# Kernel tuning notes

Hardware: AMD Instinct MI355X
Metric: run time of the kernel (lower is better)

Reference implementation:

```python
import jax, jax.numpy as jnp
import numpy as np

BETA = 1.0 - 0.01      # 1 - voltage_decay
THRESH = 1.0           # threshold_voltage; theta state is never updated in the
                       # original forward (theta1/theta2 stay at init=0), so the
                       # effective adaptive threshold is THRESH + 0 every step.
ALPHA = 2.0            # snntorch default ATan surrogate alpha

@jax.custom_vjp
def spike_fn(x):
    # Heaviside forward, ATan surrogate backward (snntorch default spike_grad)
    return (x > 0).astype(x.dtype)

def _spike_fwd(x):
    return (x > 0).astype(x.dtype), x

def _spike_bwd(x, g):
    return (g * (ALPHA / 2.0) / (1.0 + (jnp.pi / 2.0 * ALPHA * x) ** 2),)

spike_fn.defvjp(_spike_fwd, _spike_bwd)

def setup_inputs() -> dict:
    key = jax.random.key(0)
    k0, k1, k2 = jax.random.split(key, 3)
    B, T, D, H, A = 128, 32, 6400, 1000, 4
    x = jax.random.normal(k0, (B, T, D), jnp.float32)
    W1 = jax.random.normal(k1, (H, D), jnp.float32) * (1.0 / np.sqrt(D))
    b1 = jnp.zeros((H,), jnp.float32)
    W2 = jax.random.normal(k2, (A, H), jnp.float32) * (1.0 / np.sqrt(H))
    b2 = jnp.zeros((A,), jnp.float32)
    return {"x": x, "W1": W1, "b1": b1, "W2": W2, "b2": b2}

def _lif_step(mem, cur, thr):
    # snntorch Leaky, reset_mechanism='zero':
    #   reset based on PREVIOUS mem crossing threshold (detached),
    #   zeroes the whole new state (leaked mem + input) on reset step.
    reset = jax.lax.stop_gradient((mem > thr).astype(mem.dtype))
    mem_new = (BETA * mem + cur) * (1.0 - reset)
    spk = spike_fn(mem_new - thr)
    return spk, mem_new

def _snn_forward(x, W1, b1, W2, b2):
    B, T, _ = x.shape
    H, A = W1.shape[0], W2.shape[0]

    def step(carry, cur):
        mem1, mem2 = carry
        h1 = cur @ W1.T + b1                 # [B,H]
        spk1, mem1 = _lif_step(mem1, h1, THRESH)
        h2 = spk1 @ W2.T + b2                # [B,A]
        spk2, mem2 = _lif_step(mem2, h2, THRESH)
        return (mem1, mem2), spk2

    init = (jnp.zeros((B, H), x.dtype), jnp.zeros((B, A), x.dtype))
    xt = jnp.swapaxes(x, 0, 1)               # [T,B,D]
    _, spk2_rec = jax.lax.scan(step, init, xt)
    return jnp.swapaxes(spk2_rec, 0, 1)      # [B,T,A]

def reference(x, W1, b1, W2, b2):
    return _snn_forward(x, W1, b1, W2, b2)
```

## Files before the change

### kernel.cpp

```cpp
#include <hip/hip_runtime.h>
#include <hip/hip_bf16.h>

constexpr int Bn = 128;
constexpr int Tn = 32;
constexpr int Dn = 6400;
constexpr int Hn = 1000;
constexpr int An = 4;
constexpr int Mn = Bn * Tn;

typedef _Float16 half8 __attribute__((ext_vector_type(8)));
typedef float floatx4 __attribute__((ext_vector_type(4)));

__global__ __launch_bounds__(256, 4)
void gemm_split16(const float* __restrict__ X, const float* __restrict__ W1,
                  const float* __restrict__ b1, float* __restrict__ H1)
{
    constexpr int K = Dn;
    constexpr int LD = 72;
    __shared__ __align__(16) _Float16 As[2][64][LD];
    __shared__ __align__(16) _Float16 Bs[2][64][LD];

    const int tid = threadIdx.x;
    const int bm = blockIdx.x * 64;
    const int bn = blockIdx.y * 64;
    const int lane = tid & 63;
    const int wid = tid >> 6;
    const int wm = (wid & 1) * 32;
    const int wn = (wid >> 1) * 32;
    const int fr = lane & 15;
    const int fq = lane >> 4;

    const int row0 = tid >> 3;
    const int row1 = (tid + 256) >> 3;
    const int k8_0 = (tid & 7) * 8;
    const int k8_1 = k8_0;

    float4 rx[2][2], rw[2][2];
    const float zero4[4] = {0.f, 0.f, 0.f, 0.f};

    auto load_tiles = [&](int k0) {
        rx[0][0] = *(const float4*)(X + (size_t)(bm + row0) * K + k0 + k8_0);
        rx[0][1] = *(const float4*)(X + (size_t)(bm + row0) * K + k0 + k8_0 + 4);
        rx[1][0] = *(const float4*)(X + (size_t)(bm + row1) * K + k0 + k8_1);
        rx[1][1] = *(const float4*)(X + (size_t)(bm + row1) * K + k0 + k8_1 + 4);
        const int n0 = bn + row0, n1 = bn + row1;
        if (n0 < Hn) {
            rw[0][0] = *(const float4*)(W1 + (size_t)n0 * K + k0 + k8_0);
            rw[0][1] = *(const float4*)(W1 + (size_t)n0 * K + k0 + k8_0 + 4);
        } else { rw[0][0] = *(const float4*)zero4; rw[0][1] = *(const float4*)zero4; }
        if (n1 < Hn) {
            rw[1][0] = *(const float4*)(W1 + (size_t)n1 * K + k0 + k8_1);
            rw[1][1] = *(const float4*)(W1 + (size_t)n1 * K + k0 + k8_1 + 4);
        } else { rw[1][0] = *(const float4*)zero4; rw[1][1] = *(const float4*)zero4; }
    };

    load_tiles(0);

    floatx4 acc0[2][2] = {};
    floatx4 acc1[2][2] = {};

    for (int k0 = 0; k0 < K; k0 += 64) {
#pragma unroll
        for (int p = 0; p < 2; ++p) {
            const int row = p ? row1 : row0;
            const int k8 = p ? k8_1 : k8_0;
            float v[8];
            *(float4*)&v[0] = rx[p][0]; *(float4*)&v[4] = rx[p][1];
            half8 hi, lo;
#pragma unroll
            for (int j = 0; j < 8; ++j) {
                hi[j] = (_Float16)v[j];
                lo[j] = (_Float16)((v[j] - (float)hi[j]) * 4096.0f);
            }
            *(half8*)&As[0][row][k8] = hi;
            *(half8*)&As[1][row][k8] = lo;

            *(float4*)&v[0] = rw[p][0]; *(float4*)&v[4] = rw[p][1];
#pragma unroll
            for (int j = 0; j < 8; ++j) {
                hi[j] = (_Float16)v[j];
                lo[j] = (_Float16)((v[j] - (float)hi[j]) * 4096.0f);
            }
            *(half8*)&Bs[0][row][k8] = hi;
            *(half8*)&Bs[1][row][k8] = lo;
        }
        __syncthreads();

        if (k0 + 64 < K) load_tiles(k0 + 64);

#pragma unroll
        for (int c = 0; c < 2; ++c) {
            half8 ahi[2], alo[2], bhi[2], blo[2];
#pragma unroll
            for (int mt = 0; mt < 2; ++mt) {
                ahi[mt] = *(const half8*)&As[0][wm + mt * 16 + fr][c * 32 + fq * 8];
                alo[mt] = *(const half8*)&As[1][wm + mt * 16 + fr][c * 32 + fq * 8];
            }
#pragma unroll
            for (int nt = 0; nt < 2; ++nt) {
                bhi[nt] = *(const half8*)&Bs[0][wn + nt * 16 + fr][c * 32 + fq * 8];
                blo[nt] = *(const half8*)&Bs[1][wn + nt * 16 + fr][c * 32 + fq * 8];
            }
#pragma unroll
            for (int mt = 0; mt < 2; ++mt)
#pragma unroll
                for (int nt = 0; nt < 2; ++nt) {
                    acc0[mt][nt] = __builtin_amdgcn_mfma_f32_16x16x32_f16(ahi[mt], bhi[nt], acc0[mt][nt], 0, 0, 0);
                    acc1[mt][nt] = __builtin_amdgcn_mfma_f32_16x16x32_f16(ahi[mt], blo[nt], acc1[mt][nt], 0, 0, 0);
                    acc1[mt][nt] = __builtin_amdgcn_mfma_f32_16x16x32_f16(alo[mt], bhi[nt], acc1[mt][nt], 0, 0, 0);
                }
        }
        __syncthreads();
    }

#pragma unroll
    for (int nt = 0; nt < 2; ++nt) {
        const int n = bn + wn + nt * 16 + fr;
        if (n >= Hn) continue;
        const float bias = b1[n];
#pragma unroll
        for (int mt = 0; mt < 2; ++mt) {
            const int m = bm + wm + mt * 16 + fq * 4;
#pragma unroll
            for (int r = 0; r < 4; ++r)
                H1[(size_t)(m + r) * Hn + n] =
                    acc0[mt][nt][r] + acc1[mt][nt][r] * (1.0f / 4096.0f) + bias;
        }
    }
}

__global__ __launch_bounds__(1024)
void snn_scan(const float* __restrict__ H1, const float* __restrict__ W2,
              const float* __restrict__ b2, float* __restrict__ out)
{
    const int b = blockIdx.x;
    const int tid = threadIdx.x;
    const int lane = tid & 63;
    const int wid = tid >> 6;
    const bool act = (tid < Hn);

    float cur[Tn];
#pragma unroll
    for (int t = 0; t < Tn; ++t)
        cur[t] = act ? H1[((size_t)b * Tn + t) * Hn + tid] : 0.f;

    float w2[An];
#pragma unroll
    for (int a = 0; a < An; ++a)
        w2[a] = act ? W2[a * Hn + tid] : 0.f;

    __shared__ float red[16][An];
    float mem1 = 0.f;
    float mem2[An] = {0.f, 0.f, 0.f, 0.f};

    for (int t = 0; t < Tn; ++t) {
        const float reset = (mem1 > 1.0f) ? 1.0f : 0.0f;
        mem1 = (0.99f * mem1 + cur[t]) * (1.0f - reset);
        const bool spk = (mem1 > 1.0f);

        float p[An];
#pragma unroll
        for (int a = 0; a < An; ++a) p[a] = spk ? w2[a] : 0.f;

#pragma unroll
        for (int off = 32; off > 0; off >>= 1)
#pragma unroll
            for (int a = 0; a < An; ++a) p[a] += __shfl_down(p[a], off, 64);
        if (lane == 0) {
#pragma unroll
            for (int a = 0; a < An; ++a) red[wid][a] = p[a];
        }
        __syncthreads();

        if (wid == 0) {
            float q[An];
#pragma unroll
            for (int a = 0; a < An; ++a) q[a] = (lane < 16) ? red[lane][a] : 0.f;
#pragma unroll
            for (int off = 8; off > 0; off >>= 1)
#pragma unroll
                for (int a = 0; a < An; ++a) q[a] += __shfl_down(q[a], off, 64);
            if (lane == 0) {
#pragma unroll
                for (int a = 0; a < An; ++a) {
                    const float h2 = q[a] + b2[a];
                    const float reset2 = (mem2[a] > 1.0f) ? 1.0f : 0.0f;
                    const float m2 = (0.99f * mem2[a] + h2) * (1.0f - reset2);
                    mem2[a] = m2;
                    out[((size_t)b * Tn + t) * An + a] = (m2 > 1.0f) ? 1.0f : 0.0f;
                }
            }
        }
        __syncthreads();
    }
}

extern "C" void kernel_launch(void* const* d_in, const int* in_sizes, int n_in,
                              void* d_out, int out_size, void* d_ws, size_t ws_size,
                              hipStream_t stream) {
    const float* x  = (const float*)d_in[0];
    const float* W1 = (const float*)d_in[1];
    const float* b1 = (const float*)d_in[2];
    const float* W2 = (const float*)d_in[3];
    const float* b2 = (const float*)d_in[4];
    float* out = (float*)d_out;
    float* H1  = (float*)d_ws;

    dim3 grid(Mn / 64, (Hn + 63) / 64);
    gemm_split16<<<grid, 256, 0, stream>>>(x, W1, b1, H1);
    snn_scan<<<Bn, 1024, 0, stream>>>(H1, W2, b2, out);
}
```

Before: 420.9 us.

## Pre-split operands to fp16 hi/lo and stream tiles with async LDS loads

A new pre-pass kernel converts X and a padded W1 once into fp16 hi/lo arrays in workspace. The GEMM then fills LDS with XOR-swizzled tiles using global_load_lds, instead of loading fp32 and converting in every block. This removes the repeated per-tile conversion work and VALU pressure, but adds a full extra read and write pass over X. The SNN scan is also restructured: each thread first builds a spike bitmask across all timesteps, then waves reduce the W2 contributions per timestep in parallel, replacing 32 serial barrier-bound reductions. The old fused path remains as a fallback when the workspace is too small.

```diff
diff --git a/kernel.cpp b/kernel.cpp
--- a/kernel.cpp
+++ b/kernel.cpp
@@ -7,18 +7,65 @@
 constexpr int Hn = 1000;
 constexpr int An = 4;
 constexpr int Mn = Bn * Tn;
+constexpr int Npad = 1024;
 
 typedef _Float16 half8 __attribute__((ext_vector_type(8)));
+typedef _Float16 half4 __attribute__((ext_vector_type(4)));
 typedef float floatx4 __attribute__((ext_vector_type(4)));
 
+constexpr size_t H1_BYTES = (size_t)Mn * Hn * 4;
+constexpr size_t XS_BYTES = (size_t)Mn * Dn * 2;
+constexpr size_t WS_BYTES = (size_t)Npad * Dn * 2;
+constexpr size_t WS_NEEDED = H1_BYTES + 2 * XS_BYTES + 2 * WS_BYTES;
+
+__device__ __forceinline__ void async16(const void* g, void* l) {
+    __builtin_amdgcn_global_load_lds(
+        (const __attribute__((address_space(1))) void*)g,
+        (__attribute__((address_space(3))) void*)l, 16, 0, 0);
+}
+
+__global__ __launch_bounds__(256)
+void cvt_split(const float* __restrict__ X, const float* __restrict__ W1,
+               _Float16* __restrict__ Xh, _Float16* __restrict__ Xl,
+               _Float16* __restrict__ Wh, _Float16* __restrict__ Wl)
+{
+    constexpr size_t nX4 = (size_t)Mn * Dn / 4;
+    constexpr size_t nW4 = (size_t)Npad * Dn / 4;
+    const size_t i = (size_t)blockIdx.x * 256 + threadIdx.x;
+    if (i < nX4) {
+        const float4 v = ((const float4*)X)[i];
+        half4 hi, lo;
+        hi[0] = (_Float16)v.x; lo[0] = (_Float16)((v.x - (float)hi[0]) * 4096.0f);
+        hi[1] = (_Float16)v.y; lo[1] = (_Float16)((v.y - (float)hi[1]) * 4096.0f);
+        hi[2] = (_Float16)v.z; lo[2] = (_Float16)((v.z - (float)hi[2]) * 4096.0f);
+        hi[3] = (_Float16)v.w; lo[3] = (_Float16)((v.w - (float)hi[3]) * 4096.0f);
+        ((half4*)Xh)[i] = hi;
+        ((half4*)Xl)[i] = lo;
+    } else if (i < nX4 + nW4) {
+        const size_t j = i - nX4;
+        const size_t row = j / (Dn / 4);
+        float4 v = make_float4(0.f, 0.f, 0.f, 0.f);
+        if (row < Hn) v = ((const float4*)W1)[j];
+        half4 hi, lo;
+        hi[0] = (_Float16)v.x; lo[0] = (_Float16)((v.x - (float)hi[0]) * 4096.0f);
+        hi[1] = (_Float16)v.y; lo[1] = (_Float16)((v.y - (float)hi[1]) * 4096.0f);
+        hi[2] = (_Float16)v.z; lo[2] = (_Float16)((v.z - (float)hi[2]) * 4096.0f);
+        hi[3] = (_Float16)v.w; lo[3] = (_Float16)((v.w - (float)hi[3]) * 4096.0f);
+        ((half4*)Wh)[j] = hi;
+        ((half4*)Wl)[j] = lo;
+    }
+}
+
 __global__ __launch_bounds__(256, 4)
-void gemm_split16(const float* __restrict__ X, const float* __restrict__ W1,
-                  const float* __restrict__ b1, float* __restrict__ H1)
+void gemm_f16(const _Float16* __restrict__ Xh, const _Float16* __restrict__ Xl,
+              const _Float16* __restrict__ Wh, const _Float16* __restrict__ Wl,
+              const float* __restrict__ b1, float* __restrict__ H1)
 {
     constexpr int K = Dn;
-    constexpr int LD = 72;
-    __shared__ __align__(16) _Float16 As[2][64][LD];
-    __shared__ __align__(16) _Float16 Bs[2][64][LD];
+    __shared__ __align__(16) _Float16 Ah[64][64];
+    __shared__ __align__(16) _Float16 Al[64][64];
+    __shared__ __align__(16) _Float16 Bh[64][64];
+    __shared__ __align__(16) _Float16 Bl[64][64];
 
     const int tid = threadIdx.x;
     const int bm = blockIdx.x * 64;
@@ -30,10 +77,106 @@
     const int fr = lane & 15;
     const int fq = lane >> 4;
 
+    const int w16 = wid * 16;
+    const int lr = lane >> 3;
+    const int lc = lane & 7;
+    const int sw = lc ^ lr;
+
+    const size_t offA0 = (size_t)(bm + w16 + lr) * K + sw * 8;
+    const size_t offA1 = offA0 + (size_t)8 * K;
+    const size_t offB0 = (size_t)(bn + w16 + lr) * K + sw * 8;
+    const size_t offB1 = offB0 + (size_t)8 * K;
+
+    auto issue = [&](int k0) {
+        async16(Xh + offA0 + k0, &Ah[w16][0]);
+        async16(Xh + offA1 + k0, &Ah[w16 + 8][0]);
+        async16(Xl + offA0 + k0, &Al[w16][0]);
+        async16(Xl + offA1 + k0, &Al[w16 + 8][0]);
+        async16(Wh + offB0 + k0, &Bh[w16][0]);
+        async16(Wh + offB1 + k0, &Bh[w16 + 8][0]);
+        async16(Wl + offB0 + k0, &Bl[w16][0]);
+        async16(Wl + offB1 + k0, &Bl[w16 + 8][0]);
+    };
+
+    floatx4 acc0[2][2] = {};
+    floatx4 acc1[2][2] = {};
+
+    const int p0 = (0 * 4 + fq) ^ (fr & 7);
+    const int p1 = (1 * 4 + fq) ^ (fr & 7);
+    const int rA0 = wm + fr, rA1 = wm + 16 + fr;
+    const int rB0 = wn + fr, rB1 = wn + 16 + fr;
+
+    issue(0);
+    for (int k0 = 0; k0 < K; k0 += 64) {
+        __syncthreads();
+
+        half8 ahi[2][2], alo[2][2], bhi[2][2], blo[2][2];
+#pragma unroll
+        for (int c = 0; c < 2; ++c) {
+            const int o = (c ? p1 : p0) * 8;
+            ahi[c][0] = *(const half8*)&Ah[rA0][o];
+            ahi[c][1] = *(const half8*)&Ah[rA1][o];
+            alo[c][0] = *(const half8*)&Al[rA0][o];
+            alo[c][1] = *(const half8*)&Al[rA1][o];
+            bhi[c][0] = *(const half8*)&Bh[rB0][o];
+            bhi[c][1] = *(const half8*)&Bh[rB1][o];
+            blo[c][0] = *(const half8*)&Bl[rB0][o];
+            blo[c][1] = *(const half8*)&Bl[rB1][o];
+        }
+        __syncthreads();
+
+        if (k0 + 64 < K) issue(k0 + 64);
+
+#pragma unroll
+        for (int c = 0; c < 2; ++c)
+#pragma unroll
+            for (int mt = 0; mt < 2; ++mt)
+#pragma unroll
+                for (int nt = 0; nt < 2; ++nt) {
+                    acc0[mt][nt] = __builtin_amdgcn_mfma_f32_16x16x32_f16(ahi[c][mt], bhi[c][nt], acc0[mt][nt], 0, 0, 0);
+                    acc1[mt][nt] = __builtin_amdgcn_mfma_f32_16x16x32_f16(ahi[c][mt], blo[c][nt], acc1[mt][nt], 0, 0, 0);
+                    acc1[mt][nt] = __builtin_amdgcn_mfma_f32_16x16x32_f16(alo[c][mt], bhi[c][nt], acc1[mt][nt], 0, 0, 0);
+                }
+    }
+
+#pragma unroll
+    for (int nt = 0; nt < 2; ++nt) {
+        const int n = bn + wn + nt * 16 + fr;
+        if (n >= Hn) continue;
+        const float bias = b1[n];
+#pragma unroll
+        for (int mt = 0; mt < 2; ++mt) {
+            const int m = bm + wm + mt * 16 + fq * 4;
+#pragma unroll
+            for (int r = 0; r < 4; ++r)
+                H1[(size_t)(m + r) * Hn + n] =
+                    acc0[mt][nt][r] + acc1[mt][nt][r] * (1.0f / 4096.0f) + bias;
+        }
+    }
+}
+
+__global__ __launch_bounds__(256, 4)
+void gemm_fb(const float* __restrict__ X, const float* __restrict__ W1,
+             const float* __restrict__ b1, float* __restrict__ H1)
+{
+    constexpr int K = Dn;
+    constexpr int LD = 72;
+    __shared__ __align__(16) _Float16 As[2][64][LD];
+    __shared__ __align__(16) _Float16 Bs[2][64][LD];
+
+    const int tid = threadIdx.x;
+    const int bm = blockIdx.x * 64;
+    const int bn = blockIdx.y * 64;
+    const int lane = tid & 63;
+    const int wid = tid >> 6;
+    const int wm = (wid & 1) * 32;
+    const int wn = (wid >> 1) * 32;
+    const int fr = lane & 15;
+    const int fq = lane >> 4;
+
     const int row0 = tid >> 3;
     const int row1 = (tid + 256) >> 3;
     const int k8_0 = (tid & 7) * 8;
-    const int k8_1 = k8_0;
 
     float4 rx[2][2], rw[2][2];
     const float zero4[4] = {0.f, 0.f, 0.f, 0.f};
@@ -41,21 +184,20 @@
     auto load_tiles = [&](int k0) {
         rx[0][0] = *(const float4*)(X + (size_t)(bm + row0) * K + k0 + k8_0);
         rx[0][1] = *(const float4*)(X + (size_t)(bm + row0) * K + k0 + k8_0 + 4);
-        rx[1][0] = *(const float4*)(X + (size_t)(bm + row1) * K + k0 + k8_1);
-        rx[1][1] = *(const float4*)(X + (size_t)(bm + row1) * K + k0 + k8_1 + 4);
+        rx[1][0] = *(const float4*)(X + (size_t)(bm + row1) * K + k0 + k8_0);
+        rx[1][1] = *(const float4*)(X + (size_t)(bm + row1) * K + k0 + k8_0 + 4);
         const int n0 = bn + row0, n1 = bn + row1;
         if (n0 < Hn) {
             rw[0][0] = *(const float4*)(W1 + (size_t)n0 * K + k0 + k8_0);
             rw[0][1] = *(const float4*)(W1 + (size_t)n0 * K + k0 + k8_0 + 4);
         } else { rw[0][0] = *(const float4*)zero4; rw[0][1] = *(const float4*)zero4; }
         if (n1 < Hn) {
-            rw[1][0] = *(const float4*)(W1 + (size_t)n1 * K + k0 + k8_1);
-            rw[1][1] = *(const float4*)(W1 + (size_t)n1 * K + k0 + k8_1 + 4);
+            rw[1][0] = *(const float4*)(W1 + (size_t)n1 * K + k0 + k8_0);
+            rw[1][1] = *(const float4*)(W1 + (size_t)n1 * K + k0 + k8_0 + 4);
         } else { rw[1][0] = *(const float4*)zero4; rw[1][1] = *(const float4*)zero4; }
     };
 
     load_tiles(0);
-
     floatx4 acc0[2][2] = {};
     floatx4 acc1[2][2] = {};
 
@@ -63,7 +205,6 @@
 #pragma unroll
         for (int p = 0; p < 2; ++p) {
             const int row = p ? row1 : row0;
-            const int k8 = p ? k8_1 : k8_0;
             float v[8];
             *(float4*)&v[0] = rx[p][0]; *(float4*)&v[4] = rx[p][1];
             half8 hi, lo;
@@ -72,8 +213,8 @@
                 hi[j] = (_Float16)v[j];
                 lo[j] = (_Float16)((v[j] - (float)hi[j]) * 4096.0f);
             }
-            *(half8*)&As[0][row][k8] = hi;
-            *(half8*)&As[1][row][k8] = lo;
+            *(half8*)&As[0][row][k8_0] = hi;
+            *(half8*)&As[1][row][k8_0] = lo;
 
             *(float4*)&v[0] = rw[p][0]; *(float4*)&v[4] = rw[p][1];
 #pragma unroll
@@ -81,11 +222,10 @@
                 hi[j] = (_Float16)v[j];
                 lo[j] = (_Float16)((v[j] - (float)hi[j]) * 4096.0f);
             }
-            *(half8*)&Bs[0][row][k8] = hi;
-            *(half8*)&Bs[1][row][k8] = lo;
+            *(half8*)&Bs[0][row][k8_0] = hi;
+            *(half8*)&Bs[1][row][k8_0] = lo;
         }
         __syncthreads();
-
         if (k0 + 64 < K) load_tiles(k0 + 64);
 
 #pragma unroll
@@ -139,59 +279,60 @@
     const int wid = tid >> 6;
     const bool act = (tid < Hn);
 
+    __shared__ float w2s[1024][5];
+    __shared__ unsigned smask[1024];
+    __shared__ float h2s[Tn][An];
+
+#pragma unroll
+    for (int a = 0; a < An; ++a)
+        w2s[tid][a] = act ? W2[a * Hn + tid] : 0.f;
+
     float cur[Tn];
 #pragma unroll
     for (int t = 0; t < Tn; ++t)
         cur[t] = act ? H1[((size_t)b * Tn + t) * Hn + tid] : 0.f;
 
-    float w2[An];
-#pragma unroll
-    for (int a = 0; a < An; ++a)
-        w2[a] = act ? W2[a * Hn + tid] : 0.f;
-
-    __shared__ float red[16][An];
+    unsigned mask = 0;
     float mem1 = 0.f;
-    float mem2[An] = {0.f, 0.f, 0.f, 0.f};
-
+#pragma unroll
     for (int t = 0; t < Tn; ++t) {
         const float reset = (mem1 > 1.0f) ? 1.0f : 0.0f;
         mem1 = (0.99f * mem1 + cur[t]) * (1.0f - reset);
-        const bool spk = (mem1 > 1.0f);
-
-        float p[An];
-#pragma unroll
-        for (int a = 0; a < An; ++a) p[a] = spk ? w2[a] : 0.f;
-
+        if (mem1 > 1.0f) mask |= (1u << t);
+    }
+    smask[tid] = mask;
+    __syncthreads();
+
+#pragma unroll
+    for (int tt = 0; tt < 2; ++tt) {
+        const int t = wid * 2 + tt;
+        float p[An] = {0.f, 0.f, 0.f, 0.f};
+        for (int h = lane; h < 1024; h += 64) {
+            const float g = (smask[h] >> t) & 1u ? 1.0f : 0.0f;
+#pragma unroll
+            for (int a = 0; a < An; ++a) p[a] += g * w2s[h][a];
+        }
 #pragma unroll
         for (int off = 32; off > 0; off >>= 1)
 #pragma unroll
             for (int a = 0; a < An; ++a) p[a] += __shfl_down(p[a], off, 64);
         if (lane == 0) {
 #pragma unroll
-            for (int a = 0; a < An; ++a) red[wid][a] = p[a];
-        }
-        __syncthreads();
-
-        if (wid == 0) {
-            float q[An];
-#pragma unroll
-            for (int a = 0; a < An; ++a) q[a] = (lane < 16) ? red[lane][a] : 0.f;
-#pragma unroll
-            for (int off = 8; off > 0; off >>= 1)
-#pragma unroll
-                for (int a = 0; a < An; ++a) q[a] += __shfl_down(q[a], off, 64);
-            if (lane == 0) {
-#pragma unroll
-                for (int a = 0; a < An; ++a) {
-                    const float h2 = q[a] + b2[a];
-                    const float reset2 = (mem2[a] > 1.0f) ? 1.0f : 0.0f;
-                    const float m2 = (0.99f * mem2[a] + h2) * (1.0f - reset2);
-                    mem2[a] = m2;
-                    out[((size_t)b * Tn + t) * An + a] = (m2 > 1.0f) ? 1.0f : 0.0f;
-                }
-            }
-        }
-        __syncthreads();
+            for (int a = 0; a < An; ++a) h2s[t][a] = p[a];
+        }
+    }
+    __syncthreads();
+
+    if (tid < An) {
+        const float bias = b2[tid];
+        float mem2 = 0.f;
+#pragma unroll
+        for (int t = 0; t < Tn; ++t) {
+            const float h2 = h2s[t][tid] + bias;
+            const float reset = (mem2 > 1.0f) ? 1.0f : 0.0f;
+            mem2 = (0.99f * mem2 + h2) * (1.0f - reset);
+            out[((size_t)b * Tn + t) * An + tid] = (mem2 > 1.0f) ? 1.0f : 0.0f;
+        }
     }
 }
 
@@ -204,9 +345,24 @@
     const float* W2 = (const float*)d_in[3];
     const float* b2 = (const float*)d_in[4];
     float* out = (float*)d_out;
-    float* H1  = (float*)d_ws;
-
-    dim3 grid(Mn / 64, (Hn + 63) / 64);
-    gemm_split16<<<grid, 256, 0, stream>>>(x, W1, b1, H1);
+
+    char* ws = (char*)d_ws;
+    float* H1 = (float*)ws;
+
+    if (ws_size >= WS_NEEDED) {
+        _Float16* Xh = (_Float16*)(ws + H1_BYTES);
+        _Float16* Xl = (_Float16*)(ws + H1_BYTES + XS_BYTES);
+        _Float16* Wh = (_Float16*)(ws + H1_BYTES + 2 * XS_BYTES);
+        _Float16* Wl = (_Float16*)(ws + H1_BYTES + 2 * XS_BYTES + WS_BYTES);
+
+        constexpr size_t n4 = ((size_t)Mn * Dn + (size_t)Npad * Dn) / 4;
+        cvt_split<<<(unsigned)((n4 + 255) / 256), 256, 0, stream>>>(x, W1, Xh, Xl, Wh, Wl);
+
+        dim3 grid(Mn / 64, Npad / 64);
+        gemm_f16<<<grid, 256, 0, stream>>>(Xh, Xl, Wh, Wl, b1, H1);
+    } else {
+        dim3 grid(Mn / 64, (Hn + 63) / 64);
+        gemm_fb<<<grid, 256, 0, stream>>>(x, W1, b1, H1);
+    }
     snn_scan<<<Bn, 1024, 0, stream>>>(H1, W2, b2, out);
 }
```

Result: slower. 448.1 us (+6.5%).
